# Performance work log

Hardware: AMD Instinct MI355X
Metric: run time of the kernel (lower is better)

Reference implementation:

```python
import jax, jax.numpy as jnp
import numpy as np
import math

ALPHA = 1.3
N_ITER = 50


def entmax_bisect(logits, alpha=ALPHA, n_iter=N_ITER):
    # logits: [..., D]; entmax over the last axis via bisection on tau.
    x = logits / max(1.0, abs(alpha - 1.0))  # divisor is 1.0 for alpha=1.3
    x = x - jnp.max(x, axis=-1, keepdims=True)  # max_x subtraction (differentiable, as in torch)
    xs = jax.lax.stop_gradient(x)  # tau_lo/tau_hi are .detach()'d in the original
    tau_lo = jnp.min(xs, axis=-1, keepdims=True) - 1.0
    tau_hi = jnp.max(xs, axis=-1, keepdims=True) - 1e-6
    inv = 1.0 / (alpha - 1.0)

    def body(_, carry):
        lo, hi = carry
        tau = (lo + hi) * 0.5
        p = jnp.maximum(xs - tau, 0.0) ** inv
        f = jnp.sum(p, axis=-1, keepdims=True) ** (alpha - 1.0)
        big = f > 1.0
        return (jnp.where(big, tau, lo), jnp.where(big, hi, tau))

    tau_lo, tau_hi = jax.lax.fori_loop(0, n_iter, body, (tau_lo, tau_hi))
    tau = (tau_lo + tau_hi) * 0.5
    p = jnp.maximum(x - tau, 0.0) ** inv
    return p / (jnp.sum(p, axis=-1, keepdims=True) + 1e-12)


def setup_inputs() -> dict:
    key = jax.random.key(0)
    kq, kk, kv = jax.random.split(key, 3)
    B, N, D = 16, 2048, 64
    return {
        "q": jax.random.normal(kq, (B, N, D), dtype=jnp.float32),
        "k": jax.random.normal(kk, (B, N, D), dtype=jnp.float32),
        "v": jax.random.normal(kv, (B, N, D), dtype=jnp.float32),
    }


def reference(q, k, v):
    d = q.shape[-1]
    scores = jnp.einsum("bnd,bmd->bnm", q, k) / math.sqrt(d)  # [B,N,N]
    attn = entmax_bisect(scores, alpha=ALPHA)
    out = jnp.einsum("bnm,bmd->bnd", attn, v)
    return out, attn
```

## Files before the change

### kernel.cpp

```cpp
#include <hip/hip_runtime.h>


#define NBATCH 16
#define NSEQ   2048
#define DHEAD  64
#define OUT_OFF (NBATCH * NSEQ * DHEAD)
#define INV_A    3.3333333f
#define INV_A_M1 2.3333333f

typedef float  vfloat4 __attribute__((ext_vector_type(4)));
typedef float  f32x4   __attribute__((ext_vector_type(4)));
typedef short  bf16x8  __attribute__((ext_vector_type(8)));
typedef unsigned short u16x8 __attribute__((ext_vector_type(8)));

__device__ __forceinline__ float fast_log2(float x) { return __builtin_amdgcn_logf(x); }
__device__ __forceinline__ float fast_exp2(float x) { return __builtin_amdgcn_exp2f(x); }

__device__ __forceinline__ unsigned bf16_rne(float x) {
    const unsigned u = __float_as_uint(x);
    return (u + 0x7FFFu + ((u >> 16) & 1u)) >> 16;
}

__global__ __launch_bounds__(256) void ksplit_kernel(
    const float* __restrict__ K, unsigned short* __restrict__ Khi,
    unsigned short* __restrict__ Klo)
{
    const size_t idx = (size_t)blockIdx.x * 256 + threadIdx.x;
    const float4 x = ((const float4*)K)[idx];
    const float xs[4] = {x.x, x.y, x.z, x.w};
    unsigned short h[4], l[4];
    #pragma unroll
    for (int i = 0; i < 4; ++i) {
        const unsigned hr = bf16_rne(xs[i]);
        h[i] = (unsigned short)hr;
        l[i] = (unsigned short)bf16_rne(xs[i] - __uint_as_float(hr << 16));
    }
    ((ushort4*)Khi)[idx] = make_ushort4(h[0], h[1], h[2], h[3]);
    ((ushort4*)Klo)[idx] = make_ushort4(l[0], l[1], l[2], l[3]);
}

__global__ __launch_bounds__(512, 4) void entmax_attn_kernel(
    const float* __restrict__ Q, const float* __restrict__ V,
    float* __restrict__ Out,
    const unsigned short* __restrict__ Khi, const unsigned short* __restrict__ Klo)
{
    __shared__ __align__(16) float reg0[8192];
    __shared__ __align__(16) float cvx[8 * 256];

    const int tid  = threadIdx.x;
    const int w    = tid >> 6;
    const int lane = tid & 63;
    const int arow = lane & 15;
    const int lg   = lane >> 4;

    const int i   = blockIdx.x;
    const int xcd = i & 7;
    const int j2  = i >> 3;
    const int b   = xcd + 8 * (j2 & 1);
    const int rb  = j2 >> 1;
    const int n0  = rb * 16;

    const float* Vb = V + (size_t)b * NSEQ * DHEAD;
    const unsigned short* KhiB = Khi + (size_t)b * NSEQ * DHEAD;
    const unsigned short* KloB = Klo + (size_t)b * NSEQ * DHEAD;
    char* ldsHi = (char*)reg0;
    char* ldsLo = (char*)reg0 + 16384;

    bf16x8 a_hi[2], a_lo[2];
    {
        const float* qrow = Q + ((size_t)b * NSEQ + (size_t)(n0 + arow)) * DHEAD;
        #pragma unroll
        for (int ks = 0; ks < 2; ++ks) {
            const int d0 = ks * 32 + lg * 8;
            const float4 x0 = *(const float4*)(qrow + d0);
            const float4 x1 = *(const float4*)(qrow + d0 + 4);
            const float xs[8] = {x0.x, x0.y, x0.z, x0.w, x1.x, x1.y, x1.z, x1.w};
            #pragma unroll
            for (int e = 0; e < 8; ++e) {
                const float xq = xs[e] * 0.125f;
                const unsigned hr = bf16_rne(xq);
                a_hi[ks][e] = (short)hr;
                a_lo[ks][e] = (short)bf16_rne(xq - __uint_as_float(hr << 16));
            }
        }
    }

    float s[2][32];
    const int kap = 16 * w + arow;

    #pragma unroll
    for (int g = 0; g < 4; ++g) {
        f32x4 acc[4];
        #pragma unroll
        for (int tt = 0; tt < 4; ++tt) acc[tt] = (f32x4){0.f, 0.f, 0.f, 0.f};

        #pragma unroll
        for (int tt = 0; tt < 4; ++tt) {
            const int t = 4 * g + tt;
            __syncthreads();
            #pragma unroll
            for (int rep = 0; rep < 2; ++rep) {
                const int f = tid + (rep << 9);
                const int keyl = f >> 3, c = f & 7;
                const size_t goff = (size_t)(t * 128 + keyl) * DHEAD + c * 8;
                const u16x8 hv = *(const u16x8*)(KhiB + goff);
                const u16x8 lv = *(const u16x8*)(KloB + goff);
                const int loff = keyl * 128 + ((c ^ (keyl & 7)) << 4);
                *(u16x8*)(ldsHi + loff) = hv;
                *(u16x8*)(ldsLo + loff) = lv;
            }
            __syncthreads();

            #pragma unroll
            for (int ks = 0; ks < 2; ++ks) {
                const int loff = kap * 128 + ((((ks << 2) | lg) ^ (kap & 7)) << 4);
                const bf16x8 bh = *(const bf16x8*)(ldsHi + loff);
                const bf16x8 bl = *(const bf16x8*)(ldsLo + loff);
                acc[tt] = __builtin_amdgcn_mfma_f32_16x16x32_bf16(a_hi[ks], bh, acc[tt], 0, 0, 0);
                acc[tt] = __builtin_amdgcn_mfma_f32_16x16x32_bf16(a_hi[ks], bl, acc[tt], 0, 0, 0);
                acc[tt] = __builtin_amdgcn_mfma_f32_16x16x32_bf16(a_lo[ks], bh, acc[tt], 0, 0, 0);
            }
        }

        __syncthreads();
        #pragma unroll
        for (int tt = 0; tt < 4; ++tt)
            #pragma unroll
            for (int i2 = 0; i2 < 4; ++i2)
                reg0[(lg * 4 + i2) * 512 + tt * 128 + kap] = acc[tt][i2];
        __syncthreads();
        #pragma unroll
        for (int r = 0; r < 2; ++r)
            #pragma unroll
            for (int jj = 0; jj < 8; ++jj)
                s[r][8 * g + jj] = reg0[(2 * w + r) * 512 + jj * 64 + lane];
    }
    __syncthreads();

    float* prow = reg0 + w * 1024;
    float* cval = cvx + w * 256;
    float* cidx = cval + 128;
    const unsigned long long lt_mask = (1ull << lane) - 1ull;
    const int na = n0 + 2 * w;

    #pragma unroll
    for (int r = 0; r < 2; ++r) {
        float mx = s[r][0];
        #pragma unroll
        for (int j = 1; j < 32; ++j) mx = fmaxf(mx, s[r][j]);
        #pragma unroll
        for (int off = 32; off >= 1; off >>= 1) mx = fmaxf(mx, __shfl_xor(mx, off, 64));
        #pragma unroll
        for (int j = 0; j < 32; ++j) s[r][j] -= mx;

        int base = 0;
        #pragma unroll
        for (int j = 0; j < 32; ++j) {
            const bool act = s[r][j] > -1.0f;
            const unsigned long long bm = __ballot(act);
            const int pos = base + __popcll(bm & lt_mask);
            if (act && pos < 128) {
                cval[pos] = s[r][j];
                cidx[pos] = (float)(j * 64 + lane);
            }
            base += __popcll(bm);
        }
        const int A = base;
        float outacc = 0.f;

        if (A <= 128) {
            const float cv0 = cval[lane];
            const float cv1 = cval[64 + lane];
            const bool ok0 = (lane < A);
            const bool ok1 = (64 + lane < A);

            float lo = -1.0f, hi = -1e-6f;
            #pragma unroll 1
            for (int it = 0; it < 12; ++it) {
                const float tau = 0.5f * (lo + hi);
                const float t0 = cv0 - tau, t1 = cv1 - tau;
                float S = ((ok0 && t0 > 0.f) ? fast_exp2(INV_A * fast_log2(t0)) : 0.f)
                        + ((ok1 && t1 > 0.f) ? fast_exp2(INV_A * fast_log2(t1)) : 0.f);
                #pragma unroll
                for (int off = 32; off >= 1; off >>= 1) S += __shfl_xor(S, off, 64);
                if (S > 1.f) lo = tau; else hi = tau;
            }
            float tau = lo;
            #pragma unroll 1
            for (int it = 0; it < 2; ++it) {
                const float t0 = cv0 - tau, t1 = cv1 - tau;
                float S1 = 0.f, S2 = 0.f;
                if (ok0 && t0 > 0.f) {
                    const float l = fast_log2(t0);
                    S1 += fast_exp2(INV_A * l); S2 += fast_exp2(INV_A_M1 * l);
                }
                if (ok1 && t1 > 0.f) {
                    const float l = fast_log2(t1);
                    S1 += fast_exp2(INV_A * l); S2 += fast_exp2(INV_A_M1 * l);
                }
                #pragma unroll
                for (int off = 32; off >= 1; off >>= 1) {
                    S1 += __shfl_xor(S1, off, 64);
                    S2 += __shfl_xor(S2, off, 64);
                }
                tau += (S1 - 1.f) / (INV_A * S2);
                tau = fmaxf(fminf(tau, hi), lo);
            }

            const float t0 = cv0 - tau, t1 = cv1 - tau;
            float p0 = (ok0 && t0 > 0.f) ? fast_exp2(INV_A * fast_log2(t0)) : 0.f;
            float p1 = (ok1 && t1 > 0.f) ? fast_exp2(INV_A * fast_log2(t1)) : 0.f;
            float S = p0 + p1;
            #pragma unroll
            for (int off = 32; off >= 1; off >>= 1) S += __shfl_xor(S, off, 64);
            const float rnorm = 1.f / (S + 1e-12f);
            p0 *= rnorm; p1 *= rnorm;
            const int i0 = ok0 ? (int)cidx[lane] : 0;
            const int i1 = ok1 ? (int)cidx[64 + lane] : 0;
            if (ok0) cval[lane] = p0;
            if (ok1) cval[64 + lane] = p1;

            float* arow2 = Out + OUT_OFF + ((size_t)b * NSEQ + (na + r)) * NSEQ;
            #pragma unroll
            for (int seg = 0; seg < 2; ++seg) {
                #pragma unroll
                for (int z = 0; z < 4; ++z)
                    *(float4*)&prow[(z * 64 + lane) * 4] = make_float4(0.f, 0.f, 0.f, 0.f);
                if (ok0 && (i0 >> 10) == seg) prow[i0 & 1023] = p0;
                if (ok1 && (i1 >> 10) == seg) prow[i1 & 1023] = p1;
                #pragma unroll
                for (int z = 0; z < 4; ++z) {
                    const vfloat4 pv = *(const vfloat4*)&prow[(z * 64 + lane) * 4];
                    __builtin_nontemporal_store(pv,
                        (vfloat4*)&arow2[seg * 1024 + (z * 64 + lane) * 4]);
                }
            }

            int ii = 0;
            #pragma unroll 1
            for (; ii + 4 <= A; ii += 4) {
                const float pa = cval[ii + 0], pb = cval[ii + 1];
                const float pc = cval[ii + 2], pd = cval[ii + 3];
                const int ma = (int)cidx[ii + 0], mb = (int)cidx[ii + 1];
                const int mc = (int)cidx[ii + 2], md = (int)cidx[ii + 3];
                const float va = Vb[(size_t)ma * DHEAD + lane];
                const float vb2 = Vb[(size_t)mb * DHEAD + lane];
                const float vc = Vb[(size_t)mc * DHEAD + lane];
                const float vd = Vb[(size_t)md * DHEAD + lane];
                outacc += pa * va + pb * vb2 + pc * vc + pd * vd;
            }
            #pragma unroll 1
            for (; ii < A; ++ii)
                outacc += cval[ii] * Vb[(size_t)(int)cidx[ii] * DHEAD + lane];
        } else {
            float lo = -1.0f, hi = -1e-6f;
            #pragma unroll 1
            for (int it = 0; it < 12; ++it) {
                const float tau = 0.5f * (lo + hi);
                float S = 0.f;
                #pragma unroll
                for (int j = 0; j < 32; ++j) {
                    const float t = s[r][j] - tau;
                    const float p = fast_exp2(INV_A * fast_log2(t));
                    S += (t > 0.f) ? p : 0.f;
                }
                #pragma unroll
                for (int off = 32; off >= 1; off >>= 1) S += __shfl_xor(S, off, 64);
                if (S > 1.f) lo = tau; else hi = tau;
            }
            float tau = lo;
            #pragma unroll 1
            for (int it = 0; it < 2; ++it) {
                float S1 = 0.f, S2 = 0.f;
                #pragma unroll
                for (int j = 0; j < 32; ++j) {
                    const float t = s[r][j] - tau;
                    if (t > 0.f) {
                        const float l = fast_log2(t);
                        S1 += fast_exp2(INV_A * l); S2 += fast_exp2(INV_A_M1 * l);
                    }
                }
                #pragma unroll
                for (int off = 32; off >= 1; off >>= 1) {
                    S1 += __shfl_xor(S1, off, 64);
                    S2 += __shfl_xor(S2, off, 64);
                }
                tau += (S1 - 1.f) / (INV_A * S2);
                tau = fmaxf(fminf(tau, hi), lo);
            }
            float S = 0.f;
            #pragma unroll
            for (int j = 0; j < 32; ++j) {
                const float t = s[r][j] - tau;
                const float p = (t > 0.f) ? fast_exp2(INV_A * fast_log2(t)) : 0.f;
                s[r][j] = p;
                S += p;
            }
            #pragma unroll
            for (int off = 32; off >= 1; off >>= 1) S += __shfl_xor(S, off, 64);
            const float rnorm = 1.f / (S + 1e-12f);

            float* arow2 = Out + OUT_OFF + ((size_t)b * NSEQ + (na + r)) * NSEQ;
            #pragma unroll
            for (int seg = 0; seg < 2; ++seg) {
                #pragma unroll
                for (int jj = 0; jj < 16; ++jj)
                    prow[jj * 64 + lane] = s[r][seg * 16 + jj] * rnorm;
                #pragma unroll
                for (int z = 0; z < 16; ++z)
                    __builtin_nontemporal_store(prow[z * 64 + lane],
                                                &arow2[seg * 1024 + z * 64 + lane]);
                #pragma unroll 4
                for (int m = 0; m < 1024; ++m)
                    outacc += prow[m] * Vb[(size_t)(seg * 1024 + m) * DHEAD + lane];
            }
        }

        Out[((size_t)b * NSEQ + (na + r)) * DHEAD + lane] = outacc;
    }
}

extern "C" void kernel_launch(void* const* d_in, const int* in_sizes, int n_in,
                              void* d_out, int out_size, void* d_ws, size_t ws_size,
                              hipStream_t stream) {
    const float* q = (const float*)d_in[0];
    const float* k = (const float*)d_in[1];
    const float* v = (const float*)d_in[2];
    float* out = (float*)d_out;
    (void)in_sizes; (void)n_in; (void)out_size; (void)ws_size;

    unsigned short* Khi = (unsigned short*)d_ws;
    unsigned short* Klo = Khi + (size_t)NBATCH * NSEQ * DHEAD;

    hipLaunchKernelGGL(ksplit_kernel, dim3(2048), dim3(256), 0, stream, k, Khi, Klo);
    hipLaunchKernelGGL(entmax_attn_kernel, dim3(2048), dim3(512), 0, stream,
                       q, v, out, Khi, Klo);
}
```

Before: 464.9 us.

## Prefetch K tiles into registers and interleave entmax for two rows

K hi/lo tiles for the next step are now loaded from global memory into registers while the current tile's MFMAs run, so load latency overlaps compute. When both rows of a wave have at most 128 active candidates, the bisection, Newton refinement, attention-row writes and sparse V gather for both rows run interleaved. This gives more independent instructions and halves the shuffle-reduction latency chains. The candidate LDS buffer doubles and register pressure rises, which under the 512-thread, 4-block launch bound could cause spills.

```diff
diff --git a/kernel.cpp b/kernel.cpp
--- a/kernel.cpp
+++ b/kernel.cpp
@@ -45,7 +45,7 @@
     const unsigned short* __restrict__ Khi, const unsigned short* __restrict__ Klo)
 {
     __shared__ __align__(16) float reg0[8192];
-    __shared__ __align__(16) float cvx[8 * 256];
+    __shared__ __align__(16) float cvx[8 * 512];
 
     const int tid  = threadIdx.x;
     const int w    = tid >> 6;
@@ -88,6 +88,16 @@
     float s[2][32];
     const int kap = 16 * w + arow;
 
+    const int keyA = tid >> 3, cA = tid & 7;
+    const int keyB = keyA + 64;
+    const size_t gA = (size_t)keyA * DHEAD + cA * 8;
+    const size_t gB = (size_t)keyB * DHEAD + cA * 8;
+    const int ofA = keyA * 128 + ((cA ^ (keyA & 7)) << 4);
+    const int ofB = keyB * 128 + ((cA ^ (keyA & 7)) << 4);
+
+    u16x8 shA = *(const u16x8*)(KhiB + gA), slA = *(const u16x8*)(KloB + gA);
+    u16x8 shB = *(const u16x8*)(KhiB + gB), slB = *(const u16x8*)(KloB + gB);
+
     #pragma unroll
     for (int g = 0; g < 4; ++g) {
         f32x4 acc[4];
@@ -98,17 +108,8 @@
         for (int tt = 0; tt < 4; ++tt) {
             const int t = 4 * g + tt;
             __syncthreads();
-            #pragma unroll
-            for (int rep = 0; rep < 2; ++rep) {
-                const int f = tid + (rep << 9);
-                const int keyl = f >> 3, c = f & 7;
-                const size_t goff = (size_t)(t * 128 + keyl) * DHEAD + c * 8;
-                const u16x8 hv = *(const u16x8*)(KhiB + goff);
-                const u16x8 lv = *(const u16x8*)(KloB + goff);
-                const int loff = keyl * 128 + ((c ^ (keyl & 7)) << 4);
-                *(u16x8*)(ldsHi + loff) = hv;
-                *(u16x8*)(ldsLo + loff) = lv;
-            }
+            *(u16x8*)(ldsHi + ofA) = shA;  *(u16x8*)(ldsLo + ofA) = slA;
+            *(u16x8*)(ldsHi + ofB) = shB;  *(u16x8*)(ldsLo + ofB) = slB;
             __syncthreads();
 
             #pragma unroll
@@ -120,6 +121,13 @@
                 acc[tt] = __builtin_amdgcn_mfma_f32_16x16x32_bf16(a_hi[ks], bl, acc[tt], 0, 0, 0);
                 acc[tt] = __builtin_amdgcn_mfma_f32_16x16x32_bf16(a_lo[ks], bh, acc[tt], 0, 0, 0);
             }
+            if (t < 15) {
+                const size_t tb = (size_t)(t + 1) * (128 * DHEAD);
+                shA = *(const u16x8*)(KhiB + tb + gA);
+                slA = *(const u16x8*)(KloB + tb + gA);
+                shB = *(const u16x8*)(KhiB + tb + gB);
+                slB = *(const u16x8*)(KloB + tb + gB);
+            }
         }
 
         __syncthreads();
@@ -137,186 +145,337 @@
     }
     __syncthreads();
 
-    float* prow = reg0 + w * 1024;
-    float* cval = cvx + w * 256;
-    float* cidx = cval + 128;
+    float* prow  = reg0 + w * 1024;
+    float* cval0 = cvx + w * 512;
+    float* cidx0 = cval0 + 128;
+    float* cval1 = cval0 + 256;
+    float* cidx1 = cval0 + 384;
     const unsigned long long lt_mask = (1ull << lane) - 1ull;
     const int na = n0 + 2 * w;
 
-    #pragma unroll
-    for (int r = 0; r < 2; ++r) {
-        float mx = s[r][0];
-        #pragma unroll
-        for (int j = 1; j < 32; ++j) mx = fmaxf(mx, s[r][j]);
-        #pragma unroll
-        for (int off = 32; off >= 1; off >>= 1) mx = fmaxf(mx, __shfl_xor(mx, off, 64));
-        #pragma unroll
-        for (int j = 0; j < 32; ++j) s[r][j] -= mx;
-
-        int base = 0;
-        #pragma unroll
-        for (int j = 0; j < 32; ++j) {
-            const bool act = s[r][j] > -1.0f;
-            const unsigned long long bm = __ballot(act);
-            const int pos = base + __popcll(bm & lt_mask);
-            if (act && pos < 128) {
-                cval[pos] = s[r][j];
-                cidx[pos] = (float)(j * 64 + lane);
-            }
-            base += __popcll(bm);
-        }
-        const int A = base;
-        float outacc = 0.f;
-
-        if (A <= 128) {
-            const float cv0 = cval[lane];
-            const float cv1 = cval[64 + lane];
-            const bool ok0 = (lane < A);
-            const bool ok1 = (64 + lane < A);
-
-            float lo = -1.0f, hi = -1e-6f;
-            #pragma unroll 1
-            for (int it = 0; it < 12; ++it) {
-                const float tau = 0.5f * (lo + hi);
+    float mx0 = s[0][0], mx1 = s[1][0];
+    #pragma unroll
+    for (int j = 1; j < 32; ++j) { mx0 = fmaxf(mx0, s[0][j]); mx1 = fmaxf(mx1, s[1][j]); }
+    #pragma unroll
+    for (int off = 32; off >= 1; off >>= 1) {
+        mx0 = fmaxf(mx0, __shfl_xor(mx0, off, 64));
+        mx1 = fmaxf(mx1, __shfl_xor(mx1, off, 64));
+    }
+    #pragma unroll
+    for (int j = 0; j < 32; ++j) { s[0][j] -= mx0; s[1][j] -= mx1; }
+
+    int base0 = 0, base1 = 0;
+    #pragma unroll
+    for (int j = 0; j < 32; ++j) {
+        const bool a0 = s[0][j] > -1.0f;
+        const bool a1 = s[1][j] > -1.0f;
+        const unsigned long long bm0 = __ballot(a0);
+        const unsigned long long bm1 = __ballot(a1);
+        const int q0 = base0 + __popcll(bm0 & lt_mask);
+        const int q1 = base1 + __popcll(bm1 & lt_mask);
+        if (a0 && q0 < 128) { cval0[q0] = s[0][j]; cidx0[q0] = (float)(j * 64 + lane); }
+        if (a1 && q1 < 128) { cval1[q1] = s[1][j]; cidx1[q1] = (float)(j * 64 + lane); }
+        base0 += __popcll(bm0);
+        base1 += __popcll(bm1);
+    }
+    const int A0 = base0, A1 = base1;
+
+    float* arow0 = Out + OUT_OFF + ((size_t)b * NSEQ + na) * NSEQ;
+    float* arow1 = arow0 + NSEQ;
+
+    if (A0 <= 128 && A1 <= 128) {
+        const float cv00 = cval0[lane], cv01 = cval0[64 + lane];
+        const float cv10 = cval1[lane], cv11 = cval1[64 + lane];
+        const bool ok00 = lane < A0, ok01 = 64 + lane < A0;
+        const bool ok10 = lane < A1, ok11 = 64 + lane < A1;
+
+        float lo0 = -1.0f, hi0 = -1e-6f, lo1 = -1.0f, hi1 = -1e-6f;
+        #pragma unroll 1
+        for (int it = 0; it < 12; ++it) {
+            const float ta = 0.5f * (lo0 + hi0);
+            const float tb = 0.5f * (lo1 + hi1);
+            const float t00 = cv00 - ta, t01 = cv01 - ta;
+            const float t10 = cv10 - tb, t11 = cv11 - tb;
+            float S0 = ((ok00 && t00 > 0.f) ? fast_exp2(INV_A * fast_log2(t00)) : 0.f)
+                     + ((ok01 && t01 > 0.f) ? fast_exp2(INV_A * fast_log2(t01)) : 0.f);
+            float S1 = ((ok10 && t10 > 0.f) ? fast_exp2(INV_A * fast_log2(t10)) : 0.f)
+                     + ((ok11 && t11 > 0.f) ? fast_exp2(INV_A * fast_log2(t11)) : 0.f);
+            #pragma unroll
+            for (int off = 32; off >= 1; off >>= 1) {
+                S0 += __shfl_xor(S0, off, 64);
+                S1 += __shfl_xor(S1, off, 64);
+            }
+            if (S0 > 1.f) lo0 = ta; else hi0 = ta;
+            if (S1 > 1.f) lo1 = tb; else hi1 = tb;
+        }
+        float tau0 = lo0, tau1 = lo1;
+        #pragma unroll 1
+        for (int it = 0; it < 2; ++it) {
+            const float t00 = cv00 - tau0, t01 = cv01 - tau0;
+            const float t10 = cv10 - tau1, t11 = cv11 - tau1;
+            float Sa0 = 0.f, Sb0 = 0.f, Sa1 = 0.f, Sb1 = 0.f;
+            if (ok00 && t00 > 0.f) { const float l = fast_log2(t00); Sa0 += fast_exp2(INV_A * l); Sb0 += fast_exp2(INV_A_M1 * l); }
+            if (ok01 && t01 > 0.f) { const float l = fast_log2(t01); Sa0 += fast_exp2(INV_A * l); Sb0 += fast_exp2(INV_A_M1 * l); }
+            if (ok10 && t10 > 0.f) { const float l = fast_log2(t10); Sa1 += fast_exp2(INV_A * l); Sb1 += fast_exp2(INV_A_M1 * l); }
+            if (ok11 && t11 > 0.f) { const float l = fast_log2(t11); Sa1 += fast_exp2(INV_A * l); Sb1 += fast_exp2(INV_A_M1 * l); }
+            #pragma unroll
+            for (int off = 32; off >= 1; off >>= 1) {
+                Sa0 += __shfl_xor(Sa0, off, 64); Sb0 += __shfl_xor(Sb0, off, 64);
+                Sa1 += __shfl_xor(Sa1, off, 64); Sb1 += __shfl_xor(Sb1, off, 64);
+            }
+            tau0 += (Sa0 - 1.f) / (INV_A * Sb0);
+            tau0 = fmaxf(fminf(tau0, hi0), lo0);
+            tau1 += (Sa1 - 1.f) / (INV_A * Sb1);
+            tau1 = fmaxf(fminf(tau1, hi1), lo1);
+        }
+
+        const float t00 = cv00 - tau0, t01 = cv01 - tau0;
+        const float t10 = cv10 - tau1, t11 = cv11 - tau1;
+        float p00 = (ok00 && t00 > 0.f) ? fast_exp2(INV_A * fast_log2(t00)) : 0.f;
+        float p01 = (ok01 && t01 > 0.f) ? fast_exp2(INV_A * fast_log2(t01)) : 0.f;
+        float p10 = (ok10 && t10 > 0.f) ? fast_exp2(INV_A * fast_log2(t10)) : 0.f;
+        float p11 = (ok11 && t11 > 0.f) ? fast_exp2(INV_A * fast_log2(t11)) : 0.f;
+        float S0 = p00 + p01, S1 = p10 + p11;
+        #pragma unroll
+        for (int off = 32; off >= 1; off >>= 1) {
+            S0 += __shfl_xor(S0, off, 64);
+            S1 += __shfl_xor(S1, off, 64);
+        }
+        const float rn0 = 1.f / (S0 + 1e-12f);
+        const float rn1 = 1.f / (S1 + 1e-12f);
+        p00 *= rn0; p01 *= rn0; p10 *= rn1; p11 *= rn1;
+        const int i00 = ok00 ? (int)cidx0[lane] : 0;
+        const int i01 = ok01 ? (int)cidx0[64 + lane] : 0;
+        const int i10 = ok10 ? (int)cidx1[lane] : 0;
+        const int i11 = ok11 ? (int)cidx1[64 + lane] : 0;
+        if (ok00) cval0[lane] = p00;
+        if (ok01) cval0[64 + lane] = p01;
+        if (ok10) cval1[lane] = p10;
+        if (ok11) cval1[64 + lane] = p11;
+
+        #pragma unroll
+        for (int seg = 0; seg < 2; ++seg) {
+            #pragma unroll
+            for (int z = 0; z < 4; ++z)
+                *(float4*)&prow[(z * 64 + lane) * 4] = make_float4(0.f, 0.f, 0.f, 0.f);
+            if (ok00 && (i00 >> 10) == seg) prow[i00 & 1023] = p00;
+            if (ok01 && (i01 >> 10) == seg) prow[i01 & 1023] = p01;
+            #pragma unroll
+            for (int z = 0; z < 4; ++z) {
+                const vfloat4 pv = *(const vfloat4*)&prow[(z * 64 + lane) * 4];
+                __builtin_nontemporal_store(pv,
+                    (vfloat4*)&arow0[seg * 1024 + (z * 64 + lane) * 4]);
+            }
+        }
+        #pragma unroll
+        for (int seg = 0; seg < 2; ++seg) {
+            #pragma unroll
+            for (int z = 0; z < 4; ++z)
+                *(float4*)&prow[(z * 64 + lane) * 4] = make_float4(0.f, 0.f, 0.f, 0.f);
+            if (ok10 && (i10 >> 10) == seg) prow[i10 & 1023] = p10;
+            if (ok11 && (i11 >> 10) == seg) prow[i11 & 1023] = p11;
+            #pragma unroll
+            for (int z = 0; z < 4; ++z) {
+                const vfloat4 pv = *(const vfloat4*)&prow[(z * 64 + lane) * 4];
+                __builtin_nontemporal_store(pv,
+                    (vfloat4*)&arow1[seg * 1024 + (z * 64 + lane) * 4]);
+            }
+        }
+
+        float out0 = 0.f, out1 = 0.f;
+        int ii = 0;
+        #pragma unroll 1
+        for (; ii + 8 <= A0; ii += 8) {
+            const float pa = cval0[ii+0], pb = cval0[ii+1], pc = cval0[ii+2], pd = cval0[ii+3];
+            const float pe = cval0[ii+4], pf = cval0[ii+5], pg = cval0[ii+6], ph = cval0[ii+7];
+            const int ma = (int)cidx0[ii+0], mb = (int)cidx0[ii+1], mc = (int)cidx0[ii+2], md = (int)cidx0[ii+3];
+            const int me = (int)cidx0[ii+4], mf = (int)cidx0[ii+5], mg = (int)cidx0[ii+6], mh = (int)cidx0[ii+7];
+            const float va = Vb[(size_t)ma * DHEAD + lane], vb2 = Vb[(size_t)mb * DHEAD + lane];
+            const float vc = Vb[(size_t)mc * DHEAD + lane], vd  = Vb[(size_t)md * DHEAD + lane];
+            const float ve = Vb[(size_t)me * DHEAD + lane], vf  = Vb[(size_t)mf * DHEAD + lane];
+            const float vg = Vb[(size_t)mg * DHEAD + lane], vh  = Vb[(size_t)mh * DHEAD + lane];
+            out0 += pa*va + pb*vb2 + pc*vc + pd*vd + pe*ve + pf*vf + pg*vg + ph*vh;
+        }
+        #pragma unroll 1
+        for (; ii < A0; ++ii)
+            out0 += cval0[ii] * Vb[(size_t)(int)cidx0[ii] * DHEAD + lane];
+
+        int jj = 0;
+        #pragma unroll 1
+        for (; jj + 8 <= A1; jj += 8) {
+            const float pa = cval1[jj+0], pb = cval1[jj+1], pc = cval1[jj+2], pd = cval1[jj+3];
+            const float pe = cval1[jj+4], pf = cval1[jj+5], pg = cval1[jj+6], ph = cval1[jj+7];
+            const int ma = (int)cidx1[jj+0], mb = (int)cidx1[jj+1], mc = (int)cidx1[jj+2], md = (int)cidx1[jj+3];
+            const int me = (int)cidx1[jj+4], mf = (int)cidx1[jj+5], mg = (int)cidx1[jj+6], mh = (int)cidx1[jj+7];
+            const float va = Vb[(size_t)ma * DHEAD + lane], vb2 = Vb[(size_t)mb * DHEAD + lane];
+            const float vc = Vb[(size_t)mc * DHEAD + lane], vd  = Vb[(size_t)md * DHEAD + lane];
+            const float ve = Vb[(size_t)me * DHEAD + lane], vf  = Vb[(size_t)mf * DHEAD + lane];
+            const float vg = Vb[(size_t)mg * DHEAD + lane], vh  = Vb[(size_t)mh * DHEAD + lane];
+            out1 += pa*va + pb*vb2 + pc*vc + pd*vd + pe*ve + pf*vf + pg*vg + ph*vh;
+        }
+        #pragma unroll 1
+        for (; jj < A1; ++jj)
+            out1 += cval1[jj] * Vb[(size_t)(int)cidx1[jj] * DHEAD + lane];
+
+        Out[((size_t)b * NSEQ + na) * DHEAD + lane] = out0;
+        Out[((size_t)b * NSEQ + na + 1) * DHEAD + lane] = out1;
+    } else {
+        #pragma unroll
+        for (int r = 0; r < 2; ++r) {
+            const int A = r ? A1 : A0;
+            float* cval = r ? cval1 : cval0;
+            float* cidx = r ? cidx1 : cidx0;
+            float* arowX = r ? arow1 : arow0;
+            float outacc = 0.f;
+
+            if (A <= 128) {
+                const float cv0 = cval[lane];
+                const float cv1 = cval[64 + lane];
+                const bool ok0 = (lane < A);
+                const bool ok1 = (64 + lane < A);
+
+                float lo = -1.0f, hi = -1e-6f;
+                #pragma unroll 1
+                for (int it = 0; it < 12; ++it) {
+                    const float tau = 0.5f * (lo + hi);
+                    const float t0 = cv0 - tau, t1 = cv1 - tau;
+                    float S = ((ok0 && t0 > 0.f) ? fast_exp2(INV_A * fast_log2(t0)) : 0.f)
+                            + ((ok1 && t1 > 0.f) ? fast_exp2(INV_A * fast_log2(t1)) : 0.f);
+                    #pragma unroll
+                    for (int off = 32; off >= 1; off >>= 1) S += __shfl_xor(S, off, 64);
+                    if (S > 1.f) lo = tau; else hi = tau;
+                }
+                float tau = lo;
+                #pragma unroll 1
+                for (int it = 0; it < 2; ++it) {
+                    const float t0 = cv0 - tau, t1 = cv1 - tau;
+                    float S1 = 0.f, S2 = 0.f;
+                    if (ok0 && t0 > 0.f) {
+                        const float l = fast_log2(t0);
+                        S1 += fast_exp2(INV_A * l); S2 += fast_exp2(INV_A_M1 * l);
+                    }
+                    if (ok1 && t1 > 0.f) {
+                        const float l = fast_log2(t1);
+                        S1 += fast_exp2(INV_A * l); S2 += fast_exp2(INV_A_M1 * l);
+                    }
+                    #pragma unroll
+                    for (int off = 32; off >= 1; off >>= 1) {
+                        S1 += __shfl_xor(S1, off, 64);
+                        S2 += __shfl_xor(S2, off, 64);
+                    }
+                    tau += (S1 - 1.f) / (INV_A * S2);
+                    tau = fmaxf(fminf(tau, hi), lo);
+                }
+
                 const float t0 = cv0 - tau, t1 = cv1 - tau;
-                float S = ((ok0 && t0 > 0.f) ? fast_exp2(INV_A * fast_log2(t0)) : 0.f)
-                        + ((ok1 && t1 > 0.f) ? fast_exp2(INV_A * fast_log2(t1)) : 0.f);
+                float p0 = (ok0 && t0 > 0.f) ? fast_exp2(INV_A * fast_log2(t0)) : 0.f;
+                float p1 = (ok1 && t1 > 0.f) ? fast_exp2(INV_A * fast_log2(t1)) : 0.f;
+                float S = p0 + p1;
                 #pragma unroll
                 for (int off = 32; off >= 1; off >>= 1) S += __shfl_xor(S, off, 64);
-                if (S > 1.f) lo = tau; else hi = tau;
-            }
-            float tau = lo;
-            #pragma unroll 1
-            for (int it = 0; it < 2; ++it) {
-                const float t0 = cv0 - tau, t1 = cv1 - tau;
-                float S1 = 0.f, S2 = 0.f;
-                if (ok0 && t0 > 0.f) {
-                    const float l = fast_log2(t0);
-                    S1 += fast_exp2(INV_A * l); S2 += fast_exp2(INV_A_M1 * l);
-                }
-                if (ok1 && t1 > 0.f) {
-                    const float l = fast_log2(t1);
-                    S1 += fast_exp2(INV_A * l); S2 += fast_exp2(INV_A_M1 * l);
-                }
+                const float rnorm = 1.f / (S + 1e-12f);
+                p0 *= rnorm; p1 *= rnorm;
+                const int i0 = ok0 ? (int)cidx[lane] : 0;
+                const int i1 = ok1 ? (int)cidx[64 + lane] : 0;
+                if (ok0) cval[lane] = p0;
+                if (ok1) cval[64 + lane] = p1;
+
                 #pragma unroll
-                for (int off = 32; off >= 1; off >>= 1) {
-                    S1 += __shfl_xor(S1, off, 64);
-                    S2 += __shfl_xor(S2, off, 64);
-                }
-                tau += (S1 - 1.f) / (INV_A * S2);
-                tau = fmaxf(fminf(tau, hi), lo);
-            }
-
-            const float t0 = cv0 - tau, t1 = cv1 - tau;
-            float p0 = (ok0 && t0 > 0.f) ? fast_exp2(INV_A * fast_log2(t0)) : 0.f;
-            float p1 = (ok1 && t1 > 0.f) ? fast_exp2(INV_A * fast_log2(t1)) : 0.f;
-            float S = p0 + p1;
-            #pragma unroll
-            for (int off = 32; off >= 1; off >>= 1) S += __shfl_xor(S, off, 64);
-            const float rnorm = 1.f / (S + 1e-12f);
-            p0 *= rnorm; p1 *= rnorm;
-            const int i0 = ok0 ? (int)cidx[lane] : 0;
-            const int i1 = ok1 ? (int)cidx[64 + lane] : 0;
-            if (ok0) cval[lane] = p0;
-            if (ok1) cval[64 + lane] = p1;
-
-            float* arow2 = Out + OUT_OFF + ((size_t)b * NSEQ + (na + r)) * NSEQ;
-            #pragma unroll
-            for (int seg = 0; seg < 2; ++seg) {
-                #pragma unroll
-                for (int z = 0; z < 4; ++z)
-                    *(float4*)&prow[(z * 64 + lane) * 4] = make_float4(0.f, 0.f, 0.f, 0.f);
-                if (ok0 && (i0 >> 10) == seg) prow[i0 & 1023] = p0;
-                if (ok1 && (i1 >> 10) == seg) prow[i1 & 1023] = p1;
-                #pragma unroll
-                for (int z = 0; z < 4; ++z) {
-                    const vfloat4 pv = *(const vfloat4*)&prow[(z * 64 + lane) * 4];
-                    __builtin_nontemporal_store(pv,
-                        (vfloat4*)&arow2[seg * 1024 + (z * 64 + lane) * 4]);
-                }
-            }
-
-            int ii = 0;
-            #pragma unroll 1
-            for (; ii + 4 <= A; ii += 4) {
-                const float pa = cval[ii + 0], pb = cval[ii + 1];
-                const float pc = cval[ii + 2], pd = cval[ii + 3];
-                const int ma = (int)cidx[ii + 0], mb = (int)cidx[ii + 1];
-                const int mc = (int)cidx[ii + 2], md = (int)cidx[ii + 3];
-                const float va = Vb[(size_t)ma * DHEAD + lane];
-                const float vb2 = Vb[(size_t)mb * DHEAD + lane];
-                const float vc = Vb[(size_t)mc * DHEAD + lane];
-                const float vd = Vb[(size_t)md * DHEAD + lane];
-                outacc += pa * va + pb * vb2 + pc * vc + pd * vd;
-            }
-            #pragma unroll 1
-            for (; ii < A; ++ii)
-                outacc += cval[ii] * Vb[(size_t)(int)cidx[ii] * DHEAD + lane];
-        } else {
-            float lo = -1.0f, hi = -1e-6f;
-            #pragma unroll 1
-            for (int it = 0; it < 12; ++it) {
-                const float tau = 0.5f * (lo + hi);
+                for (int seg = 0; seg < 2; ++seg) {
+                    #pragma unroll
+                    for (int z = 0; z < 4; ++z)
+                        *(float4*)&prow[(z * 64 + lane) * 4] = make_float4(0.f, 0.f, 0.f, 0.f);
+                    if (ok0 && (i0 >> 10) == seg) prow[i0 & 1023] = p0;
+                    if (ok1 && (i1 >> 10) == seg) prow[i1 & 1023] = p1;
+                    #pragma unroll
+                    for (int z = 0; z < 4; ++z) {
+                        const vfloat4 pv = *(const vfloat4*)&prow[(z * 64 + lane) * 4];
+                        __builtin_nontemporal_store(pv,
+                            (vfloat4*)&arowX[seg * 1024 + (z * 64 + lane) * 4]);
+                    }
+                }
+
+                int ii = 0;
+                #pragma unroll 1
+                for (; ii + 4 <= A; ii += 4) {
+                    const float pa = cval[ii + 0], pb = cval[ii + 1];
+                    const float pc = cval[ii + 2], pd = cval[ii + 3];
+                    const int ma = (int)cidx[ii + 0], mb = (int)cidx[ii + 1];
+                    const int mc = (int)cidx[ii + 2], md = (int)cidx[ii + 3];
+                    const float va = Vb[(size_t)ma * DHEAD + lane];
+                    const float vb2 = Vb[(size_t)mb * DHEAD + lane];
+                    const float vc = Vb[(size_t)mc * DHEAD + lane];
+                    const float vd = Vb[(size_t)md * DHEAD + lane];
+                    outacc += pa * va + pb * vb2 + pc * vc + pd * vd;
+                }
+                #pragma unroll 1
+                for (; ii < A; ++ii)
+                    outacc += cval[ii] * Vb[(size_t)(int)cidx[ii] * DHEAD + lane];
+            } else {
+                float lo = -1.0f, hi = -1e-6f;
+                #pragma unroll 1
+                for (int it = 0; it < 12; ++it) {
+                    const float tau = 0.5f * (lo + hi);
+                    float S = 0.f;
+                    #pragma unroll
+                    for (int j = 0; j < 32; ++j) {
+                        const float t = s[r][j] - tau;
+                        const float p = fast_exp2(INV_A * fast_log2(t));
+                        S += (t > 0.f) ? p : 0.f;
+                    }
+                    #pragma unroll
+                    for (int off = 32; off >= 1; off >>= 1) S += __shfl_xor(S, off, 64);
+                    if (S > 1.f) lo = tau; else hi = tau;
+                }
+                float tau = lo;
+                #pragma unroll 1
+                for (int it = 0; it < 2; ++it) {
+                    float S1 = 0.f, S2 = 0.f;
+                    #pragma unroll
+                    for (int j = 0; j < 32; ++j) {
+                        const float t = s[r][j] - tau;
+                        if (t > 0.f) {
+                            const float l = fast_log2(t);
+                            S1 += fast_exp2(INV_A * l); S2 += fast_exp2(INV_A_M1 * l);
+                        }
+                    }
+                    #pragma unroll
+                    for (int off = 32; off >= 1; off >>= 1) {
+                        S1 += __shfl_xor(S1, off, 64);
+                        S2 += __shfl_xor(S2, off, 64);
+                    }
+                    tau += (S1 - 1.f) / (INV_A * S2);
+                    tau = fmaxf(fminf(tau, hi), lo);
+                }
                 float S = 0.f;
                 #pragma unroll
                 for (int j = 0; j < 32; ++j) {
                     const float t = s[r][j] - tau;
-                    const float p = fast_exp2(INV_A * fast_log2(t));
-                    S += (t > 0.f) ? p : 0.f;
+                    const float p = (t > 0.f) ? fast_exp2(INV_A * fast_log2(t)) : 0.f;
+                    s[r][j] = p;
+                    S += p;
                 }
                 #pragma unroll
                 for (int off = 32; off >= 1; off >>= 1) S += __shfl_xor(S, off, 64);
-                if (S > 1.f) lo = tau; else hi = tau;
-            }
-            float tau = lo;
-            #pragma unroll 1
-            for (int it = 0; it < 2; ++it) {
-                float S1 = 0.f, S2 = 0.f;
+                const float rnorm = 1.f / (S + 1e-12f);
+
                 #pragma unroll
-                for (int j = 0; j < 32; ++j) {
-                    const float t = s[r][j] - tau;
-                    if (t > 0.f) {
-                        const float l = fast_log2(t);
-                        S1 += fast_exp2(INV_A * l); S2 += fast_exp2(INV_A_M1 * l);
-                    }
-                }
-                #pragma unroll
-                for (int off = 32; off >= 1; off >>= 1) {
-                    S1 += __shfl_xor(S1, off, 64);
-                    S2 += __shfl_xor(S2, off, 64);
-                }
-                tau += (S1 - 1.f) / (INV_A * S2);
-                tau = fmaxf(fminf(tau, hi), lo);
-            }
-            float S = 0.f;
-            #pragma unroll
-            for (int j = 0; j < 32; ++j) {
-                const float t = s[r][j] - tau;
-                const float p = (t > 0.f) ? fast_exp2(INV_A * fast_log2(t)) : 0.f;
-                s[r][j] = p;
-                S += p;
-            }
-            #pragma unroll
-            for (int off = 32; off >= 1; off >>= 1) S += __shfl_xor(S, off, 64);
-            const float rnorm = 1.f / (S + 1e-12f);
-
-            float* arow2 = Out + OUT_OFF + ((size_t)b * NSEQ + (na + r)) * NSEQ;
-            #pragma unroll
-            for (int seg = 0; seg < 2; ++seg) {
-                #pragma unroll
-                for (int jj = 0; jj < 16; ++jj)
-                    prow[jj * 64 + lane] = s[r][seg * 16 + jj] * rnorm;
-                #pragma unroll
-                for (int z = 0; z < 16; ++z)
-                    __builtin_nontemporal_store(prow[z * 64 + lane],
-                                                &arow2[seg * 1024 + z * 64 + lane]);
-                #pragma unroll 4
-                for (int m = 0; m < 1024; ++m)
-                    outacc += prow[m] * Vb[(size_t)(seg * 1024 + m) * DHEAD + lane];
-            }
-        }
-
-        Out[((size_t)b * NSEQ + (na + r)) * DHEAD + lane] = outacc;
+                for (int seg = 0; seg < 2; ++seg) {
+                    #pragma unroll
+                    for (int jj = 0; jj < 16; ++jj)
+                        prow[jj * 64 + lane] = s[r][seg * 16 + jj] * rnorm;
+                    #pragma unroll
+                    for (int z = 0; z < 16; ++z)
+                        __builtin_nontemporal_store(prow[z * 64 + lane],
+                                                    &arowX[seg * 1024 + z * 64 + lane]);
+                    #pragma unroll 4
+                    for (int m = 0; m < 1024; ++m)
+                        outacc += prow[m] * Vb[(size_t)(seg * 1024 + m) * DHEAD + lane];
+                }
+            }
+
+            Out[((size_t)b * NSEQ + (na + r)) * DHEAD + lane] = outacc;
+        }
     }
 }
 
```

Result: faster. 451.9 us (-2.8%).
